# Performance work log

Hardware: AMD Instinct MI355X
Metric: run time of the kernel (lower is better)

## Reference

```python
import jax, jax.numpy as jnp
import numpy as np

B, N, G, E, H, R = 4, 50000, 2, 500000, 64, 16


def setup_inputs() -> dict:
    key = jax.random.key(0)
    ks = jax.random.split(key, 12)
    return {
        "pert_mask": (jax.random.uniform(ks[0], (B, N)) < 0.1).astype(jnp.float32),
        "ctx_emb": jax.random.normal(ks[1], (B, H), jnp.float32),
        "edge_src": jax.random.randint(ks[2], (G, E), 0, N, jnp.int32),
        "edge_dst": jax.random.randint(ks[3], (G, E), 0, N, jnp.int32),
        "edge_weight": jax.random.uniform(ks[4], (G, E), jnp.float32),
        "gate_u": jax.random.normal(ks[5], (G, N, R), jnp.float32) * 0.1,
        "gate_v": jax.random.normal(ks[6], (G, N, R), jnp.float32) * 0.1,
        "lin_w": jax.random.normal(ks[7], (H,), jnp.float32) * 0.1,
        "lin_b": jax.random.normal(ks[8], (H,), jnp.float32) * 0.1,
        "post_w": jax.random.normal(ks[9], (H, H), jnp.float32) * (1.0 / np.sqrt(H)),
        "post_b": jax.random.normal(ks[10], (H,), jnp.float32) * 0.1,
        "mix_w": jax.random.normal(ks[11], (H, G), jnp.float32) * 0.1,
        "mix_b": jnp.zeros((G,), jnp.float32),
    }


def reference(pert_mask, ctx_emb, edge_src, edge_dst, edge_weight,
              gate_u, gate_v, lin_w, lin_b, post_w, post_b, mix_w, mix_b):
    # h0 = Linear(1, H)(pert_mask[..., None])  -> [B, N, H]
    h0 = pert_mask[..., None] * lin_w + lin_b
    h_list = []
    for i in range(edge_src.shape[0]):  # fixed, small number of graphs
        src, dst = edge_src[i], edge_dst[i]
        # low-rank edge gate: sigmoid(<u[src], v[dst]>)  -> [E]
        gate = jax.nn.sigmoid(jnp.sum(gate_u[i][src] * gate_v[i][dst], axis=-1))
        w = edge_weight[i] * gate  # [E]
        # gather -> weight -> scatter-add, batched over B
        msg = h0[:, src, :] * w[None, :, None]  # [B, E, H]
        agg = jnp.zeros_like(h0).at[:, dst, :].add(msg)  # [B, N, H]
        h = jax.nn.relu(agg @ post_w + post_b)  # post Linear + ReLU
        h_list.append(h.mean(axis=1))  # mean over nodes -> [B, H]
    Hs = jnp.stack(h_list, axis=1)  # [B, G, H]
    wts = jax.nn.softmax(ctx_emb @ mix_w + mix_b, axis=1)[..., None]  # [B, G, 1]
    return (Hs * wts).sum(axis=1)  # [B, H]
```

## Files before the change

### kernel.cpp

```cpp
#include <hip/hip_runtime.h>

#define BB 4
#define NN 50000
#define GG 2
#define EE 500000
#define HH 64
#define RR 16

#define CVT (GG * NN)
#define PREPB ((CVT + 255) / 256)
#define PREPT (PREPB * 256)
#define ZTOT  (GG * NN + GG * BB * NN)

#define NTT   512
#define TILES 98
#define PBLK  128
#define EPB   ((EE + PBLK - 1) / PBLK)
#define CAP   72

typedef float f32x2 __attribute__((ext_vector_type(2)));

__device__ inline unsigned int pack4_fp8(float f0, float f1, float f2, float f3) {
    int w = 0;
    w = __builtin_amdgcn_cvt_pk_fp8_f32(f0, f1, w, false);
    w = __builtin_amdgcn_cvt_pk_fp8_f32(f2, f3, w, true);
    return (unsigned int)w;
}

__device__ inline float dot16_fp8(uint4 a, uint4 b) {
    const unsigned int* pa = &a.x;
    const unsigned int* pb = &b.x;
    float s = 0.f;
#pragma unroll
    for (int i = 0; i < 4; ++i) {
        f32x2 al = __builtin_amdgcn_cvt_pk_f32_fp8((int)pa[i], false);
        f32x2 ah = __builtin_amdgcn_cvt_pk_f32_fp8((int)pa[i], true);
        f32x2 bl = __builtin_amdgcn_cvt_pk_f32_fp8((int)pb[i], false);
        f32x2 bh = __builtin_amdgcn_cvt_pk_f32_fp8((int)pb[i], true);
        s = fmaf(al.x, bl.x, s);
        s = fmaf(al.y, bl.y, s);
        s = fmaf(ah.x, bh.x, s);
        s = fmaf(ah.y, bh.y, s);
    }
    return s;
}

__device__ inline unsigned int f32_to_bf16_rn(float x) {
    unsigned int u = __float_as_uint(x);
    return (u + 0x7FFFu + ((u >> 16) & 1u)) >> 16;
}

__global__ __launch_bounds__(256) void prep_kernel(
    const float* __restrict__ pert_mask, const float* __restrict__ ctx,
    const float* __restrict__ gu, const float* __restrict__ gv,
    const float* __restrict__ lin_w, const float* __restrict__ lin_b,
    const float* __restrict__ post_w, const float* __restrict__ mix_w,
    const float* __restrict__ mix_b,
    uint4* __restrict__ guh, uint4* __restrict__ gvh,
    float* __restrict__ pw, float* __restrict__ pb, float* __restrict__ wts,
    float* __restrict__ s0g ,
    float* __restrict__ out)
{
    int t = blockIdx.x * 256 + threadIdx.x;
    for (int i = t; i < ZTOT; i += PREPT)
        __builtin_nontemporal_store(0.f, &s0g[i]);
    if (t < BB * HH) out[t] = 0.f;

    if (t < CVT) {
        int n = (t >= NN) ? (t - NN) : t;
        const float4* us = (const float4*)(gu + (size_t)t * RR);
        const float4* vs = (const float4*)(gv + (size_t)t * RR);
        float4 a0 = us[0], a1 = us[1], a2 = us[2], a3 = us[3];
        uint4 ur;
        ur.x = pack4_fp8(a0.x, a0.y, a0.z, a0.w);
        ur.y = pack4_fp8(a1.x, a1.y, a1.z, a1.w);
        ur.z = pack4_fp8(a2.x, a2.y, a2.z, a2.w);
        ur.w = pack4_fp8(a3.x, a3.y, a3.z, a3.w);
        unsigned int mbits =
            ((pert_mask[0*NN + n] != 0.f) ? 0x1u        : 0u) |
            ((pert_mask[1*NN + n] != 0.f) ? 0x100u      : 0u) |
            ((pert_mask[2*NN + n] != 0.f) ? 0x10000u    : 0u) |
            ((pert_mask[3*NN + n] != 0.f) ? 0x1000000u  : 0u);
        ur.x = (ur.x & 0xFEFEFEFEu) | mbits;
        guh[t] = ur;
        float4 b0 = vs[0], b1 = vs[1], b2 = vs[2], b3 = vs[3];
        uint4 vr;
        vr.x = pack4_fp8(b0.x, b0.y, b0.z, b0.w);
        vr.y = pack4_fp8(b1.x, b1.y, b1.z, b1.w);
        vr.z = pack4_fp8(b2.x, b2.y, b2.z, b2.w);
        vr.w = pack4_fp8(b3.x, b3.y, b3.z, b3.w);
        gvh[t] = vr;
    }
    if (blockIdx.x == 0) {
        int tt = threadIdx.x;
        if (tt < HH) {
            float a = 0.f, c = 0.f;
            for (int k = 0; k < HH; ++k) {
                float w = post_w[k*HH + tt];
                a = fmaf(lin_w[k], w, a);
                c = fmaf(lin_b[k], w, c);
            }
            pw[tt] = a; pb[tt] = c;
        } else if (tt < HH + BB) {
            int b = tt - HH;
            float l0 = mix_b[0], l1 = mix_b[1];
            for (int h = 0; h < HH; ++h) {
                float cv = ctx[b*HH + h];
                l0 = fmaf(cv, mix_w[h*GG + 0], l0);
                l1 = fmaf(cv, mix_w[h*GG + 1], l1);
            }
            float m = fmaxf(l0, l1);
            float e0 = __expf(l0 - m), e1 = __expf(l1 - m);
            float inv = 1.f / (e0 + e1);
            wts[b*GG + 0] = e0 * inv;
            wts[b*GG + 1] = e1 * inv;
        }
    }
}

__device__ inline void emit_edge(
    uint4 ua, uint4 va, float w0, int d, int g,
    int* lcnt, unsigned int* __restrict__ bins, int blk,
    float* __restrict__ s0g, float* __restrict__ s1g)
{
    float dot = dot16_fp8(ua, va);
    float w = w0 / (1.f + __expf(-dot));
    unsigned int mb = (ua.x & 1u) | ((ua.x >> 7) & 2u) |
                      ((ua.x >> 14) & 4u) | ((ua.x >> 21) & 8u);
    int tt = d >> 9;
    int dl = d & (NTT - 1);
    int pos = atomicAdd(&lcnt[tt], 1);
    if (pos < CAP) {
        unsigned int rec = (f32_to_bf16_rn(w) << 16) | (mb << 9) | (unsigned)dl;
        bins[(((size_t)g * TILES + tt) * PBLK + blk) * CAP + pos] = rec;
    } else {
        atomicAdd(&s0g[g * NN + d], w);
        if (mb & 1u) atomicAdd(&s1g[((size_t)g * BB + 0) * NN + d], w);
        if (mb & 2u) atomicAdd(&s1g[((size_t)g * BB + 1) * NN + d], w);
        if (mb & 4u) atomicAdd(&s1g[((size_t)g * BB + 2) * NN + d], w);
        if (mb & 8u) atomicAdd(&s1g[((size_t)g * BB + 3) * NN + d], w);
    }
}

__global__ __launch_bounds__(256) void edge_bin_kernel(
    const int* __restrict__ esrc, const int* __restrict__ edst,
    const float* __restrict__ ewgt, const uint4* __restrict__ guh,
    const uint4* __restrict__ gvh,
    unsigned int* __restrict__ bins, int* __restrict__ counts,
    float* __restrict__ s0g, float* __restrict__ s1g)
{
    int g   = blockIdx.x & 1;
    int blk = blockIdx.x >> 1;
    __shared__ int lcnt[TILES];
    int tid = threadIdx.x;
    if (tid < TILES) lcnt[tid] = 0;
    __syncthreads();

    int base   = blk * EPB;
    int nEdges = min(EPB, EE - base);
    size_t gbase = (size_t)g * EE + base;
    int gN = g * NN;
    for (int it = tid; it < nEdges; it += 512) {
        int itB = it + 256;
        bool hB = itB < nEdges;
        int itBc = hB ? itB : it;
        int   sA  = __builtin_nontemporal_load(esrc + gbase + it);
        int   dA  = __builtin_nontemporal_load(edst + gbase + it);
        float wA  = __builtin_nontemporal_load(ewgt + gbase + it);
        int   sB  = __builtin_nontemporal_load(esrc + gbase + itBc);
        int   dB  = __builtin_nontemporal_load(edst + gbase + itBc);
        float wB  = __builtin_nontemporal_load(ewgt + gbase + itBc);
        uint4 uA = guh[gN + sA];
        uint4 vA = gvh[gN + dA];
        uint4 uB = guh[gN + sB];
        uint4 vB = gvh[gN + dB];
        emit_edge(uA, vA, wA, dA, g, lcnt, bins, blk, s0g, s1g);
        if (hB) emit_edge(uB, vB, wB, dB, g, lcnt, bins, blk, s0g, s1g);
    }
    __syncthreads();
    if (tid < TILES)
        counts[((size_t)g * TILES + tid) * PBLK + blk] = min(lcnt[tid], CAP);
}

#define P2T 1024

__global__ __launch_bounds__(P2T) void tile_node_kernel(
    const unsigned int* __restrict__ bins, const int* __restrict__ counts,
    const float* __restrict__ s0g, const float* __restrict__ s1g,
    const float* __restrict__ pw, const float* __restrict__ pb,
    const float* __restrict__ post_b, const float* __restrict__ wts,
    float* __restrict__ out)
{
    int t = blockIdx.x;
    int g = blockIdx.y;
    int n0 = t * NTT;
    int ncnt = min(NTT, NN - n0);
    __shared__ float ls[5][NTT];
    __shared__ int   lcnts[PBLK];
    __shared__ float red[4][BB * HH];
    int tid = threadIdx.x;

    if (tid < NTT) {
        if (tid < ncnt) {
            ls[0][tid] = __builtin_nontemporal_load(s0g + g * NN + n0 + tid);
#pragma unroll
            for (int b = 0; b < BB; ++b)
                ls[1 + b][tid] = __builtin_nontemporal_load(
                    s1g + ((size_t)g * BB + b) * NN + n0 + tid);
        } else {
            ls[0][tid] = 0.f; ls[1][tid] = 0.f; ls[2][tid] = 0.f;
            ls[3][tid] = 0.f; ls[4][tid] = 0.f;
        }
    }
    if (tid < PBLK)
        lcnts[tid] = __builtin_nontemporal_load(
            counts + ((size_t)g * TILES + t) * PBLK + tid);
    __syncthreads();

    int wv = tid >> 6, ln = tid & 63;
    const unsigned int* bbase = bins + ((size_t)g * TILES + t) * PBLK * CAP;
    for (int bI = wv; bI < PBLK; bI += P2T / 64) {
        int cnt = lcnts[bI];
        const unsigned int* rp = bbase + (size_t)bI * CAP;
        for (int i = ln; i < cnt; i += 64) {
            unsigned int r = __builtin_nontemporal_load(rp + i);
            float w = __uint_as_float(r & 0xFFFF0000u);
            int d = r & (NTT - 1);
            unsigned int mb = (r >> 9) & 15u;
            atomicAdd(&ls[0][d], w);
            if (mb & 1u) atomicAdd(&ls[1][d], w);
            if (mb & 2u) atomicAdd(&ls[2][d], w);
            if (mb & 4u) atomicAdd(&ls[3][d], w);
            if (mb & 8u) atomicAdd(&ls[4][d], w);
        }
    }
    __syncthreads();

    int b   = (tid >> 6) & 3;
    int sub = tid >> 8;
    int h   = tid & 63;
    float pwh = pw[h], pbh = pb[h], bias = post_b[h];
    float acc = 0.f;
    int i0 = sub * (NTT / 4);
    int i1 = min(i0 + (NTT / 4), ncnt);
    for (int i = i0; i < i1; ++i) {
        float x = fmaf(ls[1 + b][i], pwh, fmaf(ls[0][i], pbh, bias));
        acc += fmaxf(x, 0.f);
    }
    red[sub][b * HH + h] = acc;
    __syncthreads();
    if (tid < BB * HH) {
        float s = red[0][tid] + red[1][tid] + red[2][tid] + red[3][tid];
        int bb = tid >> 6;
        atomicAdd(&out[tid], s * wts[bb * GG + g] * (1.0f / NN));
    }
}

extern "C" void kernel_launch(void* const* d_in, const int* in_sizes, int n_in,
                              void* d_out, int out_size, void* d_ws, size_t ws_size,
                              hipStream_t stream) {
    const float* pert_mask = (const float*)d_in[0];
    const float* ctx       = (const float*)d_in[1];
    const int*   esrc      = (const int*)d_in[2];
    const int*   edst      = (const int*)d_in[3];
    const float* ewgt      = (const float*)d_in[4];
    const float* gu        = (const float*)d_in[5];
    const float* gv        = (const float*)d_in[6];
    const float* lin_w     = (const float*)d_in[7];
    const float* lin_b     = (const float*)d_in[8];
    const float* post_w    = (const float*)d_in[9];
    const float* post_b    = (const float*)d_in[10];
    const float* mix_w     = (const float*)d_in[11];
    const float* mix_b     = (const float*)d_in[12];
    float* out = (float*)d_out;

    float* ws = (float*)d_ws;
    float* s0g = ws;
    float* s1g = ws + 100000;
    uint4* guh = (uint4*)(ws + 500000);
    uint4* gvh = guh + 100000;
    unsigned int* bins = (unsigned int*)(ws + 1300000);
    int* counts = (int*)(bins + (size_t)GG * TILES * PBLK * CAP);
    float* pw  = (float*)(counts + GG * TILES * PBLK);
    float* pb  = pw + HH;
    float* wts = pb + HH;


    prep_kernel<<<PREPB, 256, 0, stream>>>(
        pert_mask, ctx, gu, gv, lin_w, lin_b, post_w, mix_w, mix_b,
        guh, gvh, pw, pb, wts, s0g, out);

    edge_bin_kernel<<<2 * PBLK, 256, 0, stream>>>(
        esrc, edst, ewgt, guh, gvh, bins, counts, s0g, s1g);

    dim3 tg(TILES, GG);
    tile_node_kernel<<<tg, P2T, 0, stream>>>(
        bins, counts, s0g, s1g, pw, pb, post_b, wts, out);
}
```

Baseline: 53.80 us.

## Replace dense overflow accumulators with compact overflow list scanned per tile

Removes the dense per-node s0g/s1g global arrays, which had to be zeroed in the prep kernel and read back by every tile block. Bin overflow edges are now appended to a small global list that each tile block scans and filters into shared memory. The post_w/mix_w folding moves into the tile kernel, bin writes become nontemporal, and CAP drops to 64. The risk is silently dropping edges if more than OVF_MAX overflow, and every block now pays to scan the whole overflow list.

```diff
diff --git a/kernel.cpp b/kernel.cpp
--- a/kernel.cpp
+++ b/kernel.cpp
@@ -9,14 +9,13 @@
 
 #define CVT (GG * NN)
 #define PREPB ((CVT + 255) / 256)
-#define PREPT (PREPB * 256)
-#define ZTOT  (GG * NN + GG * BB * NN)
 
 #define NTT   512
 #define TILES 98
 #define PBLK  128
 #define EPB   ((EE + PBLK - 1) / PBLK)
-#define CAP   72
+#define CAP   64
+#define OVF_MAX 8192
 
 typedef float f32x2 __attribute__((ext_vector_type(2)));
 
@@ -51,21 +50,13 @@
 }
 
 __global__ __launch_bounds__(256) void prep_kernel(
-    const float* __restrict__ pert_mask, const float* __restrict__ ctx,
+    const float* __restrict__ pert_mask,
     const float* __restrict__ gu, const float* __restrict__ gv,
-    const float* __restrict__ lin_w, const float* __restrict__ lin_b,
-    const float* __restrict__ post_w, const float* __restrict__ mix_w,
-    const float* __restrict__ mix_b,
     uint4* __restrict__ guh, uint4* __restrict__ gvh,
-    float* __restrict__ pw, float* __restrict__ pb, float* __restrict__ wts,
-    float* __restrict__ s0g ,
-    float* __restrict__ out)
+    int* __restrict__ ovf_cnt)
 {
     int t = blockIdx.x * 256 + threadIdx.x;
-    for (int i = t; i < ZTOT; i += PREPT)
-        __builtin_nontemporal_store(0.f, &s0g[i]);
-    if (t < BB * HH) out[t] = 0.f;
-
+    if (t == 0) *ovf_cnt = 0;
     if (t < CVT) {
         int n = (t >= NN) ? (t - NN) : t;
         const float4* us = (const float4*)(gu + (size_t)t * RR);
@@ -91,37 +82,12 @@
         vr.w = pack4_fp8(b3.x, b3.y, b3.z, b3.w);
         gvh[t] = vr;
     }
-    if (blockIdx.x == 0) {
-        int tt = threadIdx.x;
-        if (tt < HH) {
-            float a = 0.f, c = 0.f;
-            for (int k = 0; k < HH; ++k) {
-                float w = post_w[k*HH + tt];
-                a = fmaf(lin_w[k], w, a);
-                c = fmaf(lin_b[k], w, c);
-            }
-            pw[tt] = a; pb[tt] = c;
-        } else if (tt < HH + BB) {
-            int b = tt - HH;
-            float l0 = mix_b[0], l1 = mix_b[1];
-            for (int h = 0; h < HH; ++h) {
-                float cv = ctx[b*HH + h];
-                l0 = fmaf(cv, mix_w[h*GG + 0], l0);
-                l1 = fmaf(cv, mix_w[h*GG + 1], l1);
-            }
-            float m = fmaxf(l0, l1);
-            float e0 = __expf(l0 - m), e1 = __expf(l1 - m);
-            float inv = 1.f / (e0 + e1);
-            wts[b*GG + 0] = e0 * inv;
-            wts[b*GG + 1] = e1 * inv;
-        }
-    }
 }
 
 __device__ inline void emit_edge(
     uint4 ua, uint4 va, float w0, int d, int g,
     int* lcnt, unsigned int* __restrict__ bins, int blk,
-    float* __restrict__ s0g, float* __restrict__ s1g)
+    int* __restrict__ ovf_cnt, uint2* __restrict__ ovf)
 {
     float dot = dot16_fp8(ua, va);
     float w = w0 / (1.f + __expf(-dot));
@@ -132,13 +98,13 @@
     int pos = atomicAdd(&lcnt[tt], 1);
     if (pos < CAP) {
         unsigned int rec = (f32_to_bf16_rn(w) << 16) | (mb << 9) | (unsigned)dl;
-        bins[(((size_t)g * TILES + tt) * PBLK + blk) * CAP + pos] = rec;
+        __builtin_nontemporal_store(
+            rec, &bins[(((size_t)g * TILES + tt) * PBLK + blk) * CAP + pos]);
     } else {
-        atomicAdd(&s0g[g * NN + d], w);
-        if (mb & 1u) atomicAdd(&s1g[((size_t)g * BB + 0) * NN + d], w);
-        if (mb & 2u) atomicAdd(&s1g[((size_t)g * BB + 1) * NN + d], w);
-        if (mb & 4u) atomicAdd(&s1g[((size_t)g * BB + 2) * NN + d], w);
-        if (mb & 8u) atomicAdd(&s1g[((size_t)g * BB + 3) * NN + d], w);
+        int idx = atomicAdd(ovf_cnt, 1);
+        if (idx < OVF_MAX)
+            ovf[idx] = make_uint2((unsigned)(g * NN + d) | (mb << 20),
+                                  __float_as_uint(w));
     }
 }
 
@@ -147,13 +113,15 @@
     const float* __restrict__ ewgt, const uint4* __restrict__ guh,
     const uint4* __restrict__ gvh,
     unsigned int* __restrict__ bins, int* __restrict__ counts,
-    float* __restrict__ s0g, float* __restrict__ s1g)
+    int* __restrict__ ovf_cnt, uint2* __restrict__ ovf,
+    float* __restrict__ out)
 {
     int g   = blockIdx.x & 1;
     int blk = blockIdx.x >> 1;
     __shared__ int lcnt[TILES];
     int tid = threadIdx.x;
     if (tid < TILES) lcnt[tid] = 0;
+    if (blockIdx.x == 0 && tid < BB * HH) out[tid] = 0.f;
     __syncthreads();
 
     int base   = blk * EPB;
@@ -174,8 +142,8 @@
         uint4 vA = gvh[gN + dA];
         uint4 uB = guh[gN + sB];
         uint4 vB = gvh[gN + dB];
-        emit_edge(uA, vA, wA, dA, g, lcnt, bins, blk, s0g, s1g);
-        if (hB) emit_edge(uB, vB, wB, dB, g, lcnt, bins, blk, s0g, s1g);
+        emit_edge(uA, vA, wA, dA, g, lcnt, bins, blk, ovf_cnt, ovf);
+        if (hB) emit_edge(uB, vB, wB, dB, g, lcnt, bins, blk, ovf_cnt, ovf);
     }
     __syncthreads();
     if (tid < TILES)
@@ -186,9 +154,11 @@
 
 __global__ __launch_bounds__(P2T) void tile_node_kernel(
     const unsigned int* __restrict__ bins, const int* __restrict__ counts,
-    const float* __restrict__ s0g, const float* __restrict__ s1g,
-    const float* __restrict__ pw, const float* __restrict__ pb,
-    const float* __restrict__ post_b, const float* __restrict__ wts,
+    const float* __restrict__ ctx, const float* __restrict__ lin_w,
+    const float* __restrict__ lin_b, const float* __restrict__ post_w,
+    const float* __restrict__ post_b, const float* __restrict__ mix_w,
+    const float* __restrict__ mix_b,
+    const int* __restrict__ ovf_cnt, const uint2* __restrict__ ovf,
     float* __restrict__ out)
 {
     int t = blockIdx.x;
@@ -198,23 +168,37 @@
     __shared__ float ls[5][NTT];
     __shared__ int   lcnts[PBLK];
     __shared__ float red[4][BB * HH];
+    __shared__ float lpw[HH], lpb[HH], lwt[BB];
+    __shared__ int   s_ovfn;
     int tid = threadIdx.x;
 
-    if (tid < NTT) {
-        if (tid < ncnt) {
-            ls[0][tid] = __builtin_nontemporal_load(s0g + g * NN + n0 + tid);
-#pragma unroll
-            for (int b = 0; b < BB; ++b)
-                ls[1 + b][tid] = __builtin_nontemporal_load(
-                    s1g + ((size_t)g * BB + b) * NN + n0 + tid);
-        } else {
-            ls[0][tid] = 0.f; ls[1][tid] = 0.f; ls[2][tid] = 0.f;
-            ls[3][tid] = 0.f; ls[4][tid] = 0.f;
-        }
-    }
+    for (int i = tid; i < 5 * NTT; i += P2T) ((float*)ls)[i] = 0.f;
     if (tid < PBLK)
         lcnts[tid] = __builtin_nontemporal_load(
             counts + ((size_t)g * TILES + t) * PBLK + tid);
+    if (tid >= P2T - HH) {
+        int h = tid - (P2T - HH);
+        float a = 0.f, c = 0.f;
+        for (int k = 0; k < HH; ++k) {
+            float w = post_w[k * HH + h];
+            a = fmaf(lin_w[k], w, a);
+            c = fmaf(lin_b[k], w, c);
+        }
+        lpw[h] = a; lpb[h] = c;
+    } else if (tid >= P2T - HH - BB) {
+        int b = tid - (P2T - HH - BB);
+        float l0 = mix_b[0], l1 = mix_b[1];
+        for (int h = 0; h < HH; ++h) {
+            float cv = ctx[b * HH + h];
+            l0 = fmaf(cv, mix_w[h * GG + 0], l0);
+            l1 = fmaf(cv, mix_w[h * GG + 1], l1);
+        }
+        float m = fmaxf(l0, l1);
+        float e0 = __expf(l0 - m), e1 = __expf(l1 - m);
+        lwt[b] = ((g == 0) ? e0 : e1) / (e0 + e1);
+    } else if (tid == 0) {
+        s_ovfn = min(*ovf_cnt, OVF_MAX);
+    }
     __syncthreads();
 
     int wv = tid >> 6, ln = tid & 63;
@@ -234,12 +218,27 @@
             if (mb & 8u) atomicAdd(&ls[4][d], w);
         }
     }
+    for (int i = tid; i < s_ovfn; i += P2T) {
+        uint2 r = ovf[i];
+        int key = (int)(r.x & 0xFFFFFu);
+        int lo = g * NN + n0;
+        if (key >= lo && key < lo + ncnt) {
+            int d = key - lo;
+            unsigned int mb = (r.x >> 20) & 15u;
+            float w = __uint_as_float(r.y);
+            atomicAdd(&ls[0][d], w);
+            if (mb & 1u) atomicAdd(&ls[1][d], w);
+            if (mb & 2u) atomicAdd(&ls[2][d], w);
+            if (mb & 4u) atomicAdd(&ls[3][d], w);
+            if (mb & 8u) atomicAdd(&ls[4][d], w);
+        }
+    }
     __syncthreads();
 
     int b   = (tid >> 6) & 3;
     int sub = tid >> 8;
     int h   = tid & 63;
-    float pwh = pw[h], pbh = pb[h], bias = post_b[h];
+    float pwh = lpw[h], pbh = lpb[h], bias = post_b[h];
     float acc = 0.f;
     int i0 = sub * (NTT / 4);
     int i1 = min(i0 + (NTT / 4), ncnt);
@@ -252,7 +251,7 @@
     if (tid < BB * HH) {
         float s = red[0][tid] + red[1][tid] + red[2][tid] + red[3][tid];
         int bb = tid >> 6;
-        atomicAdd(&out[tid], s * wts[bb * GG + g] * (1.0f / NN));
+        atomicAdd(&out[tid], s * lwt[bb] * (1.0f / NN));
     }
 }
 
@@ -275,25 +274,21 @@
     float* out = (float*)d_out;
 
     float* ws = (float*)d_ws;
-    float* s0g = ws;
-    float* s1g = ws + 100000;
-    uint4* guh = (uint4*)(ws + 500000);
+    uint4* guh = (uint4*)ws;
     uint4* gvh = guh + 100000;
-    unsigned int* bins = (unsigned int*)(ws + 1300000);
+    unsigned int* bins = (unsigned int*)(ws + 800000);
     int* counts = (int*)(bins + (size_t)GG * TILES * PBLK * CAP);
-    float* pw  = (float*)(counts + GG * TILES * PBLK);
-    float* pb  = pw + HH;
-    float* wts = pb + HH;
-
+    int* ovf_cnt = counts + GG * TILES * PBLK;
+    uint2* ovf = (uint2*)(ovf_cnt + 2);
 
     prep_kernel<<<PREPB, 256, 0, stream>>>(
-        pert_mask, ctx, gu, gv, lin_w, lin_b, post_w, mix_w, mix_b,
-        guh, gvh, pw, pb, wts, s0g, out);
+        pert_mask, gu, gv, guh, gvh, ovf_cnt);
 
     edge_bin_kernel<<<2 * PBLK, 256, 0, stream>>>(
-        esrc, edst, ewgt, guh, gvh, bins, counts, s0g, s1g);
+        esrc, edst, ewgt, guh, gvh, bins, counts, ovf_cnt, ovf, out);
 
     dim3 tg(TILES, GG);
     tile_node_kernel<<<tg, P2T, 0, stream>>>(
-        bins, counts, s0g, s1g, pw, pb, post_b, wts, out);
-}
+        bins, counts, ctx, lin_w, lin_b, post_w, post_b, mix_w, mix_b,
+        ovf_cnt, ovf, out);
+}
```

Result: slower. 65.19 us (+21.2%).
